# Performance work log

Measured on AMD Instinct MI355X. Metric: run time of the kernel, lower is better.

Reference implementation:

```python
import jax, jax.numpy as jnp
import numpy as np
import math

B, S, NV, D, VD = 2, 1024, 256, 4096, 768
H, KV, HD = 32, 4, 128
REP = H // KV
THETA, YSCALE, YALPHA, YBETA = 10000.0, 40.0, 1.0, 32.0
MAXSEQ = 2048
NEG = -1e30


def _yarn_cos_sin(n_pos):
    # YaRN-scaled RoPE tables, faithful to precompute_rope_yarn
    L_full = MAXSEQ * int(YSCALE)  # max_seq_len * yarn_scale as in __init__
    inv_freq = 1.0 / THETA ** (np.arange(0, HD, 2, dtype=np.float32) / HD)
    wavelengths = 2.0 * math.pi / inv_freq
    r = L_full / wavelengths
    gamma = np.clip((r - YALPHA) / (YBETA - YALPHA), 0.0, 1.0)
    inv_freq = inv_freq * ((1.0 - gamma) / YSCALE + gamma)
    freqs = np.outer(np.arange(n_pos, dtype=np.float32), inv_freq)
    emb = np.concatenate([freqs, freqs], axis=-1) / math.sqrt(0.1 * math.log(YSCALE) + 1.0)
    return jnp.asarray(np.cos(emb), jnp.float32), jnp.asarray(np.sin(emb), jnp.float32)


def setup_inputs() -> dict:
    key = jax.random.key(0)
    ks = jax.random.split(key, 7)
    x = jax.random.normal(ks[0], (B, S, D), jnp.float32)
    vision_features = jax.random.normal(ks[1], (B, NV, VD), jnp.float32)
    wq = jax.random.normal(ks[2], (H * HD, D), jnp.float32) * 0.02
    wk = jax.random.normal(ks[3], (KV * HD, D), jnp.float32) * 0.02
    wv = jax.random.normal(ks[4], (KV * HD, D), jnp.float32) * 0.02
    wo = jax.random.normal(ks[5], (D, H * HD), jnp.float32) * 0.02
    w_vision_kv = jax.random.normal(ks[6], (2 * KV * HD, VD), jnp.float32) * 0.02
    cos, sin = _yarn_cos_sin(S + NV)
    return {"x": x, "vision_features": vision_features, "wq": wq, "wk": wk,
            "wv": wv, "wo": wo, "w_vision_kv": w_vision_kv, "cos": cos, "sin": sin}


def _rotate_half(t):
    t1, t2 = t[..., : HD // 2], t[..., HD // 2 :]
    return jnp.concatenate([-t2, t1], axis=-1)


def reference(x, vision_features, wq, wk, wv, wo, w_vision_kv, cos, sin):
    b, s, _ = x.shape
    q = (x @ wq.T).reshape(b, s, H, HD)
    k = (x @ wk.T).reshape(b, s, KV, HD)
    v = (x @ wv.T).reshape(b, s, KV, HD)
    # vision KV prefix
    vkv = vision_features @ w_vision_kv.T  # [b, nv, 2*KV*HD]
    vk, vv = jnp.split(vkv, 2, axis=-1)
    nv = vision_features.shape[1]
    vk = vk.reshape(b, nv, KV, HD)
    vv = vv.reshape(b, nv, KV, HD)
    k = jnp.concatenate([vk, k], axis=1)  # [b, kvlen, KV, HD]
    v = jnp.concatenate([vv, v], axis=1)
    kvlen = k.shape[1]
    # RoPE (positions broadcast over heads)
    cq, sq = cos[None, :s, None, :], sin[None, :s, None, :]
    ck, sk = cos[None, :kvlen, None, :], sin[None, :kvlen, None, :]
    q = q * cq + _rotate_half(q) * sq
    k = k * ck + _rotate_half(k) * sk
    # GQA without materializing repeated K/V: group q heads by kv head
    qg = q.reshape(b, s, KV, REP, HD)
    scores = jnp.einsum("bsgrd,btgd->bgrst", qg, k) * (HD ** -0.5)
    # flash-style bottom-right causal: q pos i sees kv pos j <= i + (kvlen - s)
    i = jnp.arange(s)[:, None]
    j = jnp.arange(kvlen)[None, :]
    mask = j <= i + (kvlen - s)
    scores = jnp.where(mask, scores, NEG)
    probs = jax.nn.softmax(scores, axis=-1)
    out = jnp.einsum("bgrst,btgd->bsgrd", probs, v).reshape(b, s, H * HD)
    return out @ wo.T
```

## Files before the change

### kernel.cpp

```cpp
#include <hip/hip_runtime.h>
#include <hip/hip_bf16.h>
#include <cstdint>
#include <cstddef>

typedef short bf16x8 __attribute__((ext_vector_type(8)));
typedef float f32x4 __attribute__((ext_vector_type(4)));

__device__ __forceinline__ void gload_lds16(const void* g, void* l) {
  __builtin_amdgcn_global_load_lds((__attribute__((address_space(1))) const void*)g,
                                   (__attribute__((address_space(3))) void*)l, 16, 0, 0);
}

__device__ __forceinline__ unsigned short f2bf(float f) {
  unsigned u = __builtin_bit_cast(unsigned, f);
  u += 0x7fffu + ((u >> 16) & 1u);
  return (unsigned short)(u >> 16);
}
__device__ __forceinline__ float bf2f(unsigned short h) {
  unsigned u = ((unsigned)h) << 16;
  return __builtin_bit_cast(float, u);
}

struct CastPack {
  const float* s[7];
  unsigned short* d[7];
  int n4[7];
};
__global__ void k_cast_all(CastPack p) {
  const int tid0 = blockIdx.x * blockDim.x + threadIdx.x;
  const int stride = gridDim.x * blockDim.x;
#pragma unroll 1
  for (int seg = 0; seg < 7; ++seg) {
    const float4* __restrict__ src = reinterpret_cast<const float4*>(p.s[seg]);
    ushort4* __restrict__ dst = reinterpret_cast<ushort4*>(p.d[seg]);
    const int n4 = p.n4[seg];
    for (int i = tid0; i < n4; i += stride) {
      float4 v = src[i];
      ushort4 o;
      o.x = f2bf(v.x); o.y = f2bf(v.y); o.z = f2bf(v.z); o.w = f2bf(v.w);
      dst[i] = o;
    }
  }
}

__device__ __forceinline__ void storeC(float* C, size_t i, float v) { C[i] = v; }
__device__ __forceinline__ void storeC(unsigned short* C, size_t i, float v) { C[i] = f2bf(v); }

__global__ __launch_bounds__(256) void k_gemm_qv(
    const unsigned short* __restrict__ xb,
    const unsigned short* __restrict__ wqkvb,
    unsigned short* __restrict__ qkv,
    const unsigned short* __restrict__ visb,
    const unsigned short* __restrict__ wvkvb,
    unsigned short* __restrict__ vkvb) {
  __shared__ __align__(16) unsigned short lA[128 * 64];
  __shared__ __align__(16) unsigned short lB[128 * 64];
  const int tid = threadIdx.x;
  const int w = tid >> 6, l = tid & 63;
  const int orig = (int)blockIdx.x;
  const int tile = (orig & 7) * 84 + (orig >> 3);

  const unsigned short* A;
  const unsigned short* B;
  unsigned short* C;
  int K, N, m0, n0;
  if (tile < 640) {
    A = xb; B = wqkvb; C = qkv; K = 4096; N = 5120;
    m0 = (tile & 15) * 128;
    n0 = (tile >> 4) * 128;
  } else {
    int v = tile - 640;
    A = visb; B = wvkvb; C = vkvb; K = 768; N = 1024;
    m0 = (v & 3) * 128;
    n0 = (v >> 2) * 128;
  }
  const int wm = (w >> 1) * 64, wn = (w & 1) * 64;

  f32x4 acc[4][4];
#pragma unroll
  for (int i = 0; i < 4; ++i)
#pragma unroll
    for (int j = 0; j < 4; ++j) acc[i][j] = f32x4{0.f, 0.f, 0.f, 0.f};

  char* lAc = (char*)lA;
  char* lBc = (char*)lB;

  for (int k0 = 0; k0 < K; k0 += 64) {
#pragma unroll
    for (int p = 0; p < 4; ++p) {
      int r = (w * 4 + p) * 8 + (l >> 3);
      int c = (l & 7) ^ (r & 7);
      gload_lds16(A + (size_t)(m0 + r) * K + k0 + c * 8, lAc + (w * 4 + p) * 1024);
      gload_lds16(B + (size_t)(n0 + r) * K + k0 + c * 8, lBc + (w * 4 + p) * 1024);
    }
    __syncthreads();
#pragma unroll
    for (int kk = 0; kk < 2; ++kk) {
      bf16x8 af[4], bfr[4];
#pragma unroll
      for (int i = 0; i < 4; ++i) {
        int r = wm + i * 16 + (l & 15);
        int slot = (kk * 4 + (l >> 4)) ^ (r & 7);
        af[i] = *(const bf16x8*)(lAc + r * 128 + slot * 16);
      }
#pragma unroll
      for (int j = 0; j < 4; ++j) {
        int r = wn + j * 16 + (l & 15);
        int slot = (kk * 4 + (l >> 4)) ^ (r & 7);
        bfr[j] = *(const bf16x8*)(lBc + r * 128 + slot * 16);
      }
#pragma unroll
      for (int i = 0; i < 4; ++i)
#pragma unroll
        for (int j = 0; j < 4; ++j)
          acc[i][j] = __builtin_amdgcn_mfma_f32_16x16x32_bf16(af[i], bfr[j], acc[i][j], 0, 0, 0);
    }
    __syncthreads();
  }

#pragma unroll
  for (int i = 0; i < 4; ++i)
#pragma unroll
    for (int j = 0; j < 4; ++j) {
      int row = m0 + wm + i * 16 + (l >> 4) * 4;
      int col = n0 + wn + j * 16 + (l & 15);
#pragma unroll
      for (int r = 0; r < 4; ++r)
        storeC(C, (size_t)(row + r) * N + col, acc[i][j][r]);
    }
}

template <typename OutT>
__global__ __launch_bounds__(512) void k_gemm256x128(
    const unsigned short* __restrict__ A,
    const unsigned short* __restrict__ B,
    OutT* __restrict__ C,
    int M, int N, int K) {
  __shared__ __align__(16) unsigned short lA[2][2][256][32];
  __shared__ __align__(16) unsigned short lB[2][2][128][32];
  const int tid = threadIdx.x;
  const int w = tid >> 6, l = tid & 63;
  const int wr = w >> 2, wc = w & 3;
  const int lq = l & 15, g = l >> 4;
  const int fslot = (g ^ ((lq >> 1) & 3)) << 3;

  const int gm = M >> 8, gn = N >> 7;
  const int L = (int)blockIdx.x;
  const int xcd = L & 7, slot = L >> 3;
  const int m0 = (slot % gm) * 256;
  const int n0 = (xcd * (gn >> 3) + slot / gm) * 128;

  const unsigned short* Ap = A + (size_t)m0 * K;
  const unsigned short* Bp = B + (size_t)n0 * K;

  f32x4 acc[8][2];
#pragma unroll
  for (int i = 0; i < 8; ++i)
#pragma unroll
    for (int j = 0; j < 2; ++j) acc[i][j] = f32x4{0.f, 0.f, 0.f, 0.f};

  auto stageA = [&](unsigned short* lbase, int kcol) {
#pragma unroll
    for (int p = 0; p < 2; ++p) {
      int R = w * 32 + p * 16;
      int row = R + (l >> 2);
      int cc = ((l & 3) ^ ((l >> 3) & 3)) << 3;
      gload_lds16(Ap + (size_t)row * K + kcol + cc, lbase + R * 32);
    }
  };
  auto stageB = [&](unsigned short* lbase, int kcol) {
    int R = w * 16;
    int row = R + (l >> 2);
    int cc = ((l & 3) ^ ((l >> 3) & 3)) << 3;
    gload_lds16(Bp + (size_t)row * K + kcol + cc, lbase + R * 32);
  };

  const int nt = K >> 6;

  stageB(&lB[0][0][0][0], 0);
  stageA(&lA[0][0][0][0], 0);
  stageB(&lB[0][1][0][0], 32);
  stageA(&lA[0][1][0][0], 32);
  stageB(&lB[1][0][0][0], 64);
  stageA(&lA[1][0][0][0], 64);
  asm volatile("s_waitcnt vmcnt(3)" ::: "memory");
  __builtin_amdgcn_s_barrier();

  bf16x8 bfr[2], a[8];

  for (int T = 0; T < nt; ++T) {
    const int bf = T & 1, nb = bf ^ 1;

#pragma unroll
    for (int nf = 0; nf < 2; ++nf)
      bfr[nf] = *(const bf16x8*)&lB[bf][0][wc * 32 + nf * 16 + lq][fslot];
#pragma unroll
    for (int mf = 0; mf < 8; ++mf)
      a[mf] = *(const bf16x8*)&lA[bf][0][wr * 128 + mf * 16 + lq][fslot];
    if (T + 1 < nt) {
      stageA(&lA[nb][1][0][0], ((T + 1) << 6) + 32);
      stageB(&lB[nb][1][0][0], ((T + 1) << 6) + 32);
    }
    asm volatile("s_waitcnt lgkmcnt(0)" ::: "memory");
    __builtin_amdgcn_s_setprio(1);
#pragma unroll
    for (int mf = 0; mf < 8; ++mf)
#pragma unroll
      for (int nf = 0; nf < 2; ++nf)
        acc[mf][nf] = __builtin_amdgcn_mfma_f32_16x16x32_bf16(a[mf], bfr[nf], acc[mf][nf], 0, 0, 0);
    __builtin_amdgcn_s_setprio(0);
    __builtin_amdgcn_s_barrier();

#pragma unroll
    for (int nf = 0; nf < 2; ++nf)
      bfr[nf] = *(const bf16x8*)&lB[bf][1][wc * 32 + nf * 16 + lq][fslot];
#pragma unroll
    for (int mf = 0; mf < 8; ++mf)
      a[mf] = *(const bf16x8*)&lA[bf][1][wr * 128 + mf * 16 + lq][fslot];
    if (T + 2 < nt) {
      stageA(&lA[bf][0][0][0], (T + 2) << 6);
      stageB(&lB[bf][0][0][0], (T + 2) << 6);
    }
    asm volatile("s_waitcnt lgkmcnt(0)" ::: "memory");
    __builtin_amdgcn_s_setprio(1);
#pragma unroll
    for (int mf = 0; mf < 8; ++mf)
#pragma unroll
      for (int nf = 0; nf < 2; ++nf)
        acc[mf][nf] = __builtin_amdgcn_mfma_f32_16x16x32_bf16(a[mf], bfr[nf], acc[mf][nf], 0, 0, 0);
    __builtin_amdgcn_s_setprio(0);
    if (T < nt - 2)
      asm volatile("s_waitcnt vmcnt(3)" ::: "memory");
    else if (T == nt - 2)
      asm volatile("s_waitcnt vmcnt(0)" ::: "memory");
    __builtin_amdgcn_s_barrier();
  }

#pragma unroll
  for (int mf = 0; mf < 8; ++mf)
#pragma unroll
    for (int nf = 0; nf < 2; ++nf) {
      int row = m0 + wr * 128 + mf * 16 + g * 4;
      int col = n0 + wc * 32 + nf * 16 + lq;
#pragma unroll
      for (int r = 0; r < 4; ++r)
        storeC(C, (size_t)(row + r) * N + col, acc[mf][nf][r]);
    }
}

__global__ void k_post(const unsigned short* __restrict__ qkv,
                       const unsigned short* __restrict__ vkv,
                       const float* __restrict__ cosT, const float* __restrict__ sinT,
                       unsigned short* __restrict__ k_all,
                       unsigned short* __restrict__ v_t) {
  int idx = blockIdx.x * blockDim.x + threadIdx.x;
  if (idx < 655360) {
    int i = idx;
    int d0 = i & 63;
    int t = (i >> 6) % 1280;
    int bg = i / (64 * 1280);
    int b = bg >> 2, g = bg & 3;
    float a, bb;
    if (t < 256) {
      const unsigned short* src = vkv + (size_t)(b * 256 + t) * 1024 + g * 128;
      a = bf2f(src[d0]); bb = bf2f(src[d0 + 64]);
    } else {
      const unsigned short* src = qkv + (size_t)(b * 1024 + t - 256) * 5120 + 4096 + g * 128;
      a = bf2f(src[d0]); bb = bf2f(src[d0 + 64]);
    }
    float c0 = cosT[t * 128 + d0], s0 = sinT[t * 128 + d0];
    float c1 = cosT[t * 128 + d0 + 64], s1 = sinT[t * 128 + d0 + 64];
    unsigned short* dst = k_all + ((size_t)bg * 1280 + t) * 128;
    dst[d0] = f2bf(a * c0 - bb * s0);
    dst[d0 + 64] = f2bf(bb * c1 + a * s1);
  } else {
    int i = idx - 655360;
    int t = i % 1280;
    int d = (i / 1280) & 127;
    int bg = i / (1280 * 128);
    int b = bg >> 2, g = bg & 3;
    unsigned short v;
    if (t < 256) v = vkv[(size_t)(b * 256 + t) * 1024 + 512 + g * 128 + d];
    else         v = qkv[(size_t)(b * 1024 + t - 256) * 5120 + 4608 + g * 128 + d];
    v_t[(size_t)bg * 128 * 1280 + (size_t)d * 1280 + t] = v;
  }
}

__global__ __launch_bounds__(256) void k_attn(
    const unsigned short* __restrict__ qr,
    const unsigned short* __restrict__ k_all,
    const unsigned short* __restrict__ v_t,
    const float* __restrict__ cosT, const float* __restrict__ sinT,
    unsigned short* __restrict__ attn) {
  __shared__ __align__(16) unsigned short lK[2][64 * 128];
  __shared__ __align__(16) unsigned short lV[2][128 * 64];
  __shared__ __align__(16) unsigned short lPT[4][16][72];

  const int tid = threadIdx.x, w = tid >> 6, l = tid & 63;
  const int lq = l & 15, g = l >> 4;
  const int qpair = blockIdx.x;
  const int h = blockIdx.y, b = blockIdx.z;
  const int bg = b * 4 + (h >> 3);
  const unsigned short* kg = k_all + (size_t)bg * 1280 * 128;
  const unsigned short* vg = v_t + (size_t)bg * 128 * 1280;

  char* lKc = (char*)lK;
  char* lVc = (char*)lV;
  char* pbuf = (char*)&lPT[w][0][0];

  auto stage = [&](int t0, int bufsel) {
#pragma unroll
    for (int p = 0; p < 4; ++p) {
      int r = (w * 4 + p) * 4 + (l >> 4);
      int c = (l & 15) ^ (r & 7);
      gload_lds16(kg + (size_t)(t0 + r) * 128 + c * 8,
                  lKc + bufsel * 16384 + (w * 4 + p) * 1024);
    }
#pragma unroll
    for (int p = 0; p < 4; ++p) {
      int d = (w * 4 + p) * 8 + (l >> 3);
      int c = (l & 7) ^ (d & 7);
      gload_lds16(vg + (size_t)d * 1280 + t0 + c * 8,
                  lVc + bufsel * 16384 + (w * 4 + p) * 1024);
    }
  };

  int buf = 0;
#pragma unroll 1
  for (int half = 0; half < 2; ++half) {
    const int qb = (half ? (15 - qpair) : qpair) * 64;
    const int qrow_l = qb + w * 16 + lq;
    const int nIter = (qb + 320) >> 6;

    bf16x8 aq[4];
    {
      int row = qb + w * 16 + lq;
      const unsigned short* p = qr + (size_t)(b * 1024 + row) * 5120 + h * 128 + g * 8;
      bf16x8 r0 = *(const bf16x8*)(p);
      bf16x8 r1 = *(const bf16x8*)(p + 32);
      bf16x8 r2 = *(const bf16x8*)(p + 64);
      bf16x8 r3 = *(const bf16x8*)(p + 96);
      const float* cp = cosT + (size_t)row * 128;
      const float* sp = sinT + (size_t)row * 128;
      const float sc = 0.08838834764831845f;
#pragma unroll
      for (int j = 0; j < 8; ++j) {
        int d0 = g * 8 + j;
        float a0 = bf2f((unsigned short)r0[j]), b0 = bf2f((unsigned short)r2[j]);
        aq[0][j] = (short)f2bf((a0 * cp[d0] - b0 * sp[d0]) * sc);
        aq[2][j] = (short)f2bf((b0 * cp[d0 + 64] + a0 * sp[d0 + 64]) * sc);
        int d1 = 32 + g * 8 + j;
        float a1 = bf2f((unsigned short)r1[j]), b1 = bf2f((unsigned short)r3[j]);
        aq[1][j] = (short)f2bf((a1 * cp[d1] - b1 * sp[d1]) * sc);
        aq[3][j] = (short)f2bf((b1 * cp[d1 + 64] + a1 * sp[d1 + 64]) * sc);
      }
    }

    f32x4 o[8];
#pragma unroll
    for (int i = 0; i < 8; ++i) o[i] = f32x4{0.f, 0.f, 0.f, 0.f};
    float mr = -1e30f;
    float lrp = 0.f;

    stage(0, buf);
    __syncthreads();

    for (int it = 0; it < nIter; ++it) {
      const int t0 = it << 6;
      if (it + 1 < nIter) stage(t0 + 64, buf ^ 1);

      const char* kbase = lKc + buf * 16384;
      const char* vbase = lVc + buf * 16384;

      f32x4 sT[4];
#pragma unroll
      for (int sub = 0; sub < 4; ++sub) {
        f32x4 s4 = {0.f, 0.f, 0.f, 0.f};
        int krow = sub * 16 + lq;
        const char* kb = kbase + krow * 256;
#pragma unroll
        for (int kk = 0; kk < 4; ++kk) {
          int slot = (kk * 4 + g) ^ (krow & 7);
          bf16x8 kf = *(const bf16x8*)(kb + slot * 16);
          s4 = __builtin_amdgcn_mfma_f32_16x16x32_bf16(kf, aq[kk], s4, 0, 0, 0);
        }
        sT[sub] = s4;
      }

      if (t0 + 63 > qb + w * 16 + 256) {
#pragma unroll
        for (int sub = 0; sub < 4; ++sub)
#pragma unroll
          for (int r = 0; r < 4; ++r) {
            int t = t0 + sub * 16 + 4 * g + r;
            if (t > qrow_l + 256) sT[sub][r] = -1e30f;
          }
      }

      float pm = fmaxf(fmaxf(fmaxf(sT[0][0], sT[0][1]), fmaxf(sT[0][2], sT[0][3])),
                       fmaxf(fmaxf(sT[1][0], sT[1][1]), fmaxf(sT[1][2], sT[1][3])));
      pm = fmaxf(pm, fmaxf(fmaxf(fmaxf(sT[2][0], sT[2][1]), fmaxf(sT[2][2], sT[2][3])),
                           fmaxf(fmaxf(sT[3][0], sT[3][1]), fmaxf(sT[3][2], sT[3][3]))));
      pm = fmaxf(pm, __shfl_xor(pm, 16));
      pm = fmaxf(pm, __shfl_xor(pm, 32));

      if (!__all(pm <= mr + 8.0f)) {
        float mnew = fmaxf(mr, pm);
        float scl = __expf(mr - mnew);
        mr = mnew;
        lrp *= scl;
        float s0 = __shfl(scl, 4 * g + 0);
        float s1 = __shfl(scl, 4 * g + 1);
        float s2 = __shfl(scl, 4 * g + 2);
        float s3 = __shfl(scl, 4 * g + 3);
#pragma unroll
        for (int cs = 0; cs < 8; ++cs) {
          o[cs][0] *= s0; o[cs][1] *= s1; o[cs][2] *= s2; o[cs][3] *= s3;
        }
      }

#pragma unroll
      for (int sub = 0; sub < 4; ++sub) {
        float p0 = __expf(sT[sub][0] - mr);
        float p1 = __expf(sT[sub][1] - mr);
        float p2 = __expf(sT[sub][2] - mr);
        float p3 = __expf(sT[sub][3] - mr);
        lrp += (p0 + p1) + (p2 + p3);
        unsigned pk0, pk1;
        asm("v_cvt_pk_bf16_f32 %0, %1, %2" : "=v"(pk0) : "v"(p0), "v"(p1));
        asm("v_cvt_pk_bf16_f32 %0, %1, %2" : "=v"(pk1) : "v"(p2), "v"(p3));
        int c = (2 * sub + (g >> 1)) ^ (lq & 7);
        *(uint2*)(pbuf + lq * 144 + c * 16 + (g & 1) * 8) = make_uint2(pk0, pk1);
      }

      asm volatile("s_waitcnt lgkmcnt(0)" ::: "memory");

      bf16x8 pa0 = *(const bf16x8*)(pbuf + lq * 144 + ((g ^ (lq & 7)) * 16));
      bf16x8 pa1 = *(const bf16x8*)(pbuf + lq * 144 + (((4 + g) ^ (lq & 7)) * 16));

#pragma unroll
      for (int cs = 0; cs < 8; ++cs) {
        int drow = cs * 16 + lq;
        const char* vb = vbase + drow * 128;
        int s0i = g ^ (drow & 7);
        int s1i = (4 + g) ^ (drow & 7);
        bf16x8 v0 = *(const bf16x8*)(vb + s0i * 16);
        bf16x8 v1 = *(const bf16x8*)(vb + s1i * 16);
        o[cs] = __builtin_amdgcn_mfma_f32_16x16x32_bf16(pa0, v0, o[cs], 0, 0, 0);
        o[cs] = __builtin_amdgcn_mfma_f32_16x16x32_bf16(pa1, v1, o[cs], 0, 0, 0);
      }

      __syncthreads();
      buf ^= 1;
    }

    lrp += __shfl_xor(lrp, 16);
    lrp += __shfl_xor(lrp, 32);
    float inv = 1.0f / lrp;
    float invr[4];
    invr[0] = __shfl(inv, 4 * g + 0);
    invr[1] = __shfl(inv, 4 * g + 1);
    invr[2] = __shfl(inv, 4 * g + 2);
    invr[3] = __shfl(inv, 4 * g + 3);
#pragma unroll
    for (int cs = 0; cs < 8; ++cs)
#pragma unroll
      for (int r = 0; r < 4; ++r) {
        int row = qb + w * 16 + 4 * g + r;
        attn[(size_t)(b * 1024 + row) * 4096 + h * 128 + cs * 16 + lq] =
            f2bf(o[cs][r] * invr[r]);
      }
  }
}

extern "C" void kernel_launch(void* const* d_in, const int* in_sizes, int n_in,
                              void* d_out, int out_size, void* d_ws, size_t ws_size,
                              hipStream_t stream) {
  const float* x    = (const float*)d_in[0];
  const float* vis  = (const float*)d_in[1];
  const float* wq   = (const float*)d_in[2];
  const float* wk   = (const float*)d_in[3];
  const float* wv   = (const float*)d_in[4];
  const float* wo   = (const float*)d_in[5];
  const float* wvkv = (const float*)d_in[6];
  const float* cosT = (const float*)d_in[7];
  const float* sinT = (const float*)d_in[8];
  float* out = (float*)d_out;
  char* ws = (char*)d_ws;

  size_t off = 0;
  auto alloc = [&](size_t b) { size_t r = off; off += (b + 255) & ~(size_t)255; return r; };
  unsigned short* wqkvb = (unsigned short*)(ws + alloc((size_t)5120 * 4096 * 2));
  unsigned short* wob   = (unsigned short*)(ws + alloc((size_t)4096 * 4096 * 2));
  unsigned short* wvkvb = (unsigned short*)(ws + alloc((size_t)1024 * 768 * 2));
  unsigned short* visb  = (unsigned short*)(ws + alloc((size_t)512 * 768 * 2));
  unsigned short* xb    = (unsigned short*)(ws + alloc((size_t)2048 * 4096 * 2));
  unsigned short* qkv   = (unsigned short*)(ws + alloc((size_t)2048 * 5120 * 2));
  unsigned short* vkvb  = (unsigned short*)(ws + alloc((size_t)512 * 1024 * 2));
  unsigned short* kall  = (unsigned short*)(ws + alloc((size_t)8 * 1280 * 128 * 2));
  unsigned short* vt    = (unsigned short*)(ws + alloc((size_t)8 * 128 * 1280 * 2));
  unsigned short* attnb = xb;
  if (ws_size < off) return;

  CastPack cp;
  cp.s[0] = x;    cp.d[0] = xb;                           cp.n4[0] = 2048 * 4096 / 4;
  cp.s[1] = wq;   cp.d[1] = wqkvb;                        cp.n4[1] = 4096 * 4096 / 4;
  cp.s[2] = wk;   cp.d[2] = wqkvb + (size_t)4096 * 4096;  cp.n4[2] = 512 * 4096 / 4;
  cp.s[3] = wv;   cp.d[3] = wqkvb + (size_t)4608 * 4096;  cp.n4[3] = 512 * 4096 / 4;
  cp.s[4] = wo;   cp.d[4] = wob;                          cp.n4[4] = 4096 * 4096 / 4;
  cp.s[5] = wvkv; cp.d[5] = wvkvb;                        cp.n4[5] = 1024 * 768 / 4;
  cp.s[6] = vis;  cp.d[6] = visb;                         cp.n4[6] = 512 * 768 / 4;
  k_cast_all<<<dim3(2048), dim3(256), 0, stream>>>(cp);

  k_gemm_qv<<<dim3(672), dim3(256), 0, stream>>>(xb, wqkvb, qkv, visb, wvkvb, vkvb);

  k_post<<<dim3(7680), dim3(256), 0, stream>>>(qkv, vkvb, cosT, sinT, kall, vt);

  k_attn<<<dim3(8, 32, 2), dim3(256), 0, stream>>>(qkv, kall, vt, cosT, sinT, attnb);

  k_gemm256x128<float><<<dim3(256), dim3(512), 0, stream>>>(attnb, wob, out, 2048, 4096, 4096);
}
```

Baseline: 305.0 us.

## Share double-buffered 128x128 GEMM core across QKV and output projections

Adds a shared 128x128-tile GEMM routine with a split-K-half, double-buffered LDS pipeline built on async global-to-LDS loads, s_setprio and explicit vmcnt waits. The QKV/vision GEMM moves from its single-buffered loop with a full sync per k-step onto this routine. The output projection moves from 256x128 tiles with 512 threads to 128x128 tiles with 256 threads, giving 512 blocks for better occupancy and CU balance. Smaller tiles increase operand reloads from global memory for the output GEMM.

```diff
diff --git a/kernel.cpp b/kernel.cpp
--- a/kernel.cpp
+++ b/kernel.cpp
@@ -46,6 +46,107 @@
 __device__ __forceinline__ void storeC(float* C, size_t i, float v) { C[i] = v; }
 __device__ __forceinline__ void storeC(unsigned short* C, size_t i, float v) { C[i] = f2bf(v); }
 
+template <typename OutT>
+__device__ __forceinline__ void gemm128_run(
+    const unsigned short* __restrict__ Ap,
+    const unsigned short* __restrict__ Bp,
+    OutT* __restrict__ C, int K, int ldC, int m0, int n0,
+    unsigned short (&lA)[2][2][128][32], unsigned short (&lB)[2][2][128][32]) {
+  const int tid = threadIdx.x;
+  const int w = tid >> 6, l = tid & 63;
+  const int wr = w >> 1, wc = w & 1;
+  const int lq = l & 15, g = l >> 4;
+  const int fslot = (g ^ ((lq >> 1) & 3)) << 3;
+
+  f32x4 acc[4][4];
+#pragma unroll
+  for (int i = 0; i < 4; ++i)
+#pragma unroll
+    for (int j = 0; j < 4; ++j) acc[i][j] = f32x4{0.f, 0.f, 0.f, 0.f};
+
+  auto stageH = [&](const unsigned short* gbase, unsigned short* lbase, int kcol) {
+#pragma unroll
+    for (int p = 0; p < 2; ++p) {
+      int R = w * 32 + p * 16;
+      int row = R + (l >> 2);
+      int cc = ((l & 3) ^ ((l >> 3) & 3)) << 3;
+      gload_lds16(gbase + (size_t)row * K + kcol + cc, lbase + R * 32);
+    }
+  };
+
+  const int nt = K >> 6;
+
+  stageH(Bp, &lB[0][0][0][0], 0);
+  stageH(Ap, &lA[0][0][0][0], 0);
+  stageH(Bp, &lB[0][1][0][0], 32);
+  stageH(Ap, &lA[0][1][0][0], 32);
+  stageH(Bp, &lB[1][0][0][0], 64);
+  stageH(Ap, &lA[1][0][0][0], 64);
+  asm volatile("s_waitcnt vmcnt(4)" ::: "memory");
+  __builtin_amdgcn_s_barrier();
+
+  bf16x8 a[4], bq[4];
+
+  for (int T = 0; T < nt; ++T) {
+    const int bf = T & 1, nb = bf ^ 1;
+
+#pragma unroll
+    for (int i = 0; i < 4; ++i)
+      a[i] = *(const bf16x8*)&lA[bf][0][wr * 64 + i * 16 + lq][fslot];
+#pragma unroll
+    for (int j = 0; j < 4; ++j)
+      bq[j] = *(const bf16x8*)&lB[bf][0][wc * 64 + j * 16 + lq][fslot];
+    if (T + 1 < nt) {
+      stageH(Ap, &lA[nb][1][0][0], ((T + 1) << 6) + 32);
+      stageH(Bp, &lB[nb][1][0][0], ((T + 1) << 6) + 32);
+    }
+    asm volatile("s_waitcnt lgkmcnt(0)" ::: "memory");
+    __builtin_amdgcn_s_setprio(1);
+#pragma unroll
+    for (int i = 0; i < 4; ++i)
+#pragma unroll
+      for (int j = 0; j < 4; ++j)
+        acc[i][j] = __builtin_amdgcn_mfma_f32_16x16x32_bf16(a[i], bq[j], acc[i][j], 0, 0, 0);
+    __builtin_amdgcn_s_setprio(0);
+    __builtin_amdgcn_s_barrier();
+
+#pragma unroll
+    for (int i = 0; i < 4; ++i)
+      a[i] = *(const bf16x8*)&lA[bf][1][wr * 64 + i * 16 + lq][fslot];
+#pragma unroll
+    for (int j = 0; j < 4; ++j)
+      bq[j] = *(const bf16x8*)&lB[bf][1][wc * 64 + j * 16 + lq][fslot];
+    if (T + 2 < nt) {
+      stageH(Ap, &lA[bf][0][0][0], (T + 2) << 6);
+      stageH(Bp, &lB[bf][0][0][0], (T + 2) << 6);
+    }
+    asm volatile("s_waitcnt lgkmcnt(0)" ::: "memory");
+    __builtin_amdgcn_s_setprio(1);
+#pragma unroll
+    for (int i = 0; i < 4; ++i)
+#pragma unroll
+      for (int j = 0; j < 4; ++j)
+        acc[i][j] = __builtin_amdgcn_mfma_f32_16x16x32_bf16(a[i], bq[j], acc[i][j], 0, 0, 0);
+    __builtin_amdgcn_s_setprio(0);
+    if (T < nt - 2)
+      asm volatile("s_waitcnt vmcnt(4)" ::: "memory");
+    else if (T == nt - 2)
+      asm volatile("s_waitcnt vmcnt(0)" ::: "memory");
+    __builtin_amdgcn_s_barrier();
+  }
+
+#pragma unroll
+  for (int i = 0; i < 4; ++i)
+#pragma unroll
+    for (int j = 0; j < 4; ++j) {
+      int row = m0 + wr * 64 + i * 16 + g * 4;
+      int col = n0 + wc * 64 + j * 16 + lq;
+#pragma unroll
+      for (int r = 0; r < 4; ++r)
+        storeC(C, (size_t)(row + r) * ldC + col, acc[i][j][r]);
+    }
+}
+
 __global__ __launch_bounds__(256) void k_gemm_qv(
     const unsigned short* __restrict__ xb,
     const unsigned short* __restrict__ wqkvb,
@@ -53,199 +154,36 @@
     const unsigned short* __restrict__ visb,
     const unsigned short* __restrict__ wvkvb,
     unsigned short* __restrict__ vkvb) {
-  __shared__ __align__(16) unsigned short lA[128 * 64];
-  __shared__ __align__(16) unsigned short lB[128 * 64];
-  const int tid = threadIdx.x;
-  const int w = tid >> 6, l = tid & 63;
+  __shared__ __align__(16) unsigned short lA[2][2][128][32];
+  __shared__ __align__(16) unsigned short lB[2][2][128][32];
   const int orig = (int)blockIdx.x;
   const int tile = (orig & 7) * 84 + (orig >> 3);
-
-  const unsigned short* A;
-  const unsigned short* B;
-  unsigned short* C;
-  int K, N, m0, n0;
   if (tile < 640) {
-    A = xb; B = wqkvb; C = qkv; K = 4096; N = 5120;
-    m0 = (tile & 15) * 128;
-    n0 = (tile >> 4) * 128;
+    int m0 = (tile & 15) * 128;
+    int n0 = (tile >> 4) * 128;
+    gemm128_run<unsigned short>(xb + (size_t)m0 * 4096, wqkvb + (size_t)n0 * 4096,
+                                qkv, 4096, 5120, m0, n0, lA, lB);
   } else {
     int v = tile - 640;
-    A = visb; B = wvkvb; C = vkvb; K = 768; N = 1024;
-    m0 = (v & 3) * 128;
-    n0 = (v >> 2) * 128;
+    int m0 = (v & 3) * 128;
+    int n0 = (v >> 2) * 128;
+    gemm128_run<unsigned short>(visb + (size_t)m0 * 768, wvkvb + (size_t)n0 * 768,
+                                vkvb, 768, 1024, m0, n0, lA, lB);
   }
-  const int wm = (w >> 1) * 64, wn = (w & 1) * 64;
-
-  f32x4 acc[4][4];
-#pragma unroll
-  for (int i = 0; i < 4; ++i)
-#pragma unroll
-    for (int j = 0; j < 4; ++j) acc[i][j] = f32x4{0.f, 0.f, 0.f, 0.f};
-
-  char* lAc = (char*)lA;
-  char* lBc = (char*)lB;
-
-  for (int k0 = 0; k0 < K; k0 += 64) {
-#pragma unroll
-    for (int p = 0; p < 4; ++p) {
-      int r = (w * 4 + p) * 8 + (l >> 3);
-      int c = (l & 7) ^ (r & 7);
-      gload_lds16(A + (size_t)(m0 + r) * K + k0 + c * 8, lAc + (w * 4 + p) * 1024);
-      gload_lds16(B + (size_t)(n0 + r) * K + k0 + c * 8, lBc + (w * 4 + p) * 1024);
-    }
-    __syncthreads();
-#pragma unroll
-    for (int kk = 0; kk < 2; ++kk) {
-      bf16x8 af[4], bfr[4];
-#pragma unroll
-      for (int i = 0; i < 4; ++i) {
-        int r = wm + i * 16 + (l & 15);
-        int slot = (kk * 4 + (l >> 4)) ^ (r & 7);
-        af[i] = *(const bf16x8*)(lAc + r * 128 + slot * 16);
-      }
-#pragma unroll
-      for (int j = 0; j < 4; ++j) {
-        int r = wn + j * 16 + (l & 15);
-        int slot = (kk * 4 + (l >> 4)) ^ (r & 7);
-        bfr[j] = *(const bf16x8*)(lBc + r * 128 + slot * 16);
-      }
-#pragma unroll
-      for (int i = 0; i < 4; ++i)
-#pragma unroll
-        for (int j = 0; j < 4; ++j)
-          acc[i][j] = __builtin_amdgcn_mfma_f32_16x16x32_bf16(af[i], bfr[j], acc[i][j], 0, 0, 0);
-    }
-    __syncthreads();
-  }
-
-#pragma unroll
-  for (int i = 0; i < 4; ++i)
-#pragma unroll
-    for (int j = 0; j < 4; ++j) {
-      int row = m0 + wm + i * 16 + (l >> 4) * 4;
-      int col = n0 + wn + j * 16 + (l & 15);
-#pragma unroll
-      for (int r = 0; r < 4; ++r)
-        storeC(C, (size_t)(row + r) * N + col, acc[i][j][r]);
-    }
-}
-
-template <typename OutT>
-__global__ __launch_bounds__(512) void k_gemm256x128(
+}
+
+__global__ __launch_bounds__(256) void k_gemm_o(
     const unsigned short* __restrict__ A,
     const unsigned short* __restrict__ B,
-    OutT* __restrict__ C,
-    int M, int N, int K) {
-  __shared__ __align__(16) unsigned short lA[2][2][256][32];
+    float* __restrict__ C) {
+  __shared__ __align__(16) unsigned short lA[2][2][128][32];
   __shared__ __align__(16) unsigned short lB[2][2][128][32];
-  const int tid = threadIdx.x;
-  const int w = tid >> 6, l = tid & 63;
-  const int wr = w >> 2, wc = w & 3;
-  const int lq = l & 15, g = l >> 4;
-  const int fslot = (g ^ ((lq >> 1) & 3)) << 3;
-
-  const int gm = M >> 8, gn = N >> 7;
   const int L = (int)blockIdx.x;
   const int xcd = L & 7, slot = L >> 3;
-  const int m0 = (slot % gm) * 256;
-  const int n0 = (xcd * (gn >> 3) + slot / gm) * 128;
-
-  const unsigned short* Ap = A + (size_t)m0 * K;
-  const unsigned short* Bp = B + (size_t)n0 * K;
-
-  f32x4 acc[8][2];
-#pragma unroll
-  for (int i = 0; i < 8; ++i)
-#pragma unroll
-    for (int j = 0; j < 2; ++j) acc[i][j] = f32x4{0.f, 0.f, 0.f, 0.f};
-
-  auto stageA = [&](unsigned short* lbase, int kcol) {
-#pragma unroll
-    for (int p = 0; p < 2; ++p) {
-      int R = w * 32 + p * 16;
-      int row = R + (l >> 2);
-      int cc = ((l & 3) ^ ((l >> 3) & 3)) << 3;
-      gload_lds16(Ap + (size_t)row * K + kcol + cc, lbase + R * 32);
-    }
-  };
-  auto stageB = [&](unsigned short* lbase, int kcol) {
-    int R = w * 16;
-    int row = R + (l >> 2);
-    int cc = ((l & 3) ^ ((l >> 3) & 3)) << 3;
-    gload_lds16(Bp + (size_t)row * K + kcol + cc, lbase + R * 32);
-  };
-
-  const int nt = K >> 6;
-
-  stageB(&lB[0][0][0][0], 0);
-  stageA(&lA[0][0][0][0], 0);
-  stageB(&lB[0][1][0][0], 32);
-  stageA(&lA[0][1][0][0], 32);
-  stageB(&lB[1][0][0][0], 64);
-  stageA(&lA[1][0][0][0], 64);
-  asm volatile("s_waitcnt vmcnt(3)" ::: "memory");
-  __builtin_amdgcn_s_barrier();
-
-  bf16x8 bfr[2], a[8];
-
-  for (int T = 0; T < nt; ++T) {
-    const int bf = T & 1, nb = bf ^ 1;
-
-#pragma unroll
-    for (int nf = 0; nf < 2; ++nf)
-      bfr[nf] = *(const bf16x8*)&lB[bf][0][wc * 32 + nf * 16 + lq][fslot];
-#pragma unroll
-    for (int mf = 0; mf < 8; ++mf)
-      a[mf] = *(const bf16x8*)&lA[bf][0][wr * 128 + mf * 16 + lq][fslot];
-    if (T + 1 < nt) {
-      stageA(&lA[nb][1][0][0], ((T + 1) << 6) + 32);
-      stageB(&lB[nb][1][0][0], ((T + 1) << 6) + 32);
-    }
-    asm volatile("s_waitcnt lgkmcnt(0)" ::: "memory");
-    __builtin_amdgcn_s_setprio(1);
-#pragma unroll
-    for (int mf = 0; mf < 8; ++mf)
-#pragma unroll
-      for (int nf = 0; nf < 2; ++nf)
-        acc[mf][nf] = __builtin_amdgcn_mfma_f32_16x16x32_bf16(a[mf], bfr[nf], acc[mf][nf], 0, 0, 0);
-    __builtin_amdgcn_s_setprio(0);
-    __builtin_amdgcn_s_barrier();
-
-#pragma unroll
-    for (int nf = 0; nf < 2; ++nf)
-      bfr[nf] = *(const bf16x8*)&lB[bf][1][wc * 32 + nf * 16 + lq][fslot];
-#pragma unroll
-    for (int mf = 0; mf < 8; ++mf)
-      a[mf] = *(const bf16x8*)&lA[bf][1][wr * 128 + mf * 16 + lq][fslot];
-    if (T + 2 < nt) {
-      stageA(&lA[bf][0][0][0], (T + 2) << 6);
-      stageB(&lB[bf][0][0][0], (T + 2) << 6);
-    }
-    asm volatile("s_waitcnt lgkmcnt(0)" ::: "memory");
-    __builtin_amdgcn_s_setprio(1);
-#pragma unroll
-    for (int mf = 0; mf < 8; ++mf)
-#pragma unroll
-      for (int nf = 0; nf < 2; ++nf)
-        acc[mf][nf] = __builtin_amdgcn_mfma_f32_16x16x32_bf16(a[mf], bfr[nf], acc[mf][nf], 0, 0, 0);
-    __builtin_amdgcn_s_setprio(0);
-    if (T < nt - 2)
-      asm volatile("s_waitcnt vmcnt(3)" ::: "memory");
-    else if (T == nt - 2)
-      asm volatile("s_waitcnt vmcnt(0)" ::: "memory");
-    __builtin_amdgcn_s_barrier();
-  }
-
-#pragma unroll
-  for (int mf = 0; mf < 8; ++mf)
-#pragma unroll
-    for (int nf = 0; nf < 2; ++nf) {
-      int row = m0 + wr * 128 + mf * 16 + g * 4;
-      int col = n0 + wc * 32 + nf * 16 + lq;
-#pragma unroll
-      for (int r = 0; r < 4; ++r)
-        storeC(C, (size_t)(row + r) * N + col, acc[mf][nf][r]);
-    }
+  const int m0 = (slot & 15) * 128;
+  const int n0 = (xcd * 4 + (slot >> 4)) * 128;
+  gemm128_run<float>(A + (size_t)m0 * 4096, B + (size_t)n0 * 4096,
+                     C, 4096, 4096, m0, n0, lA, lB);
 }
 
 __global__ void k_post(const unsigned short* __restrict__ qkv,
@@ -518,5 +456,5 @@
 
   k_attn<<<dim3(8, 32, 2), dim3(256), 0, stream>>>(qkv, kall, vt, cosT, sinT, attnb);
 
-  k_gemm256x128<float><<<dim3(256), dim3(512), 0, stream>>>(attnb, wob, out, 2048, 4096, 4096);
-}
+  k_gemm_o<<<dim3(512), dim3(256), 0, stream>>>(attnb, wob, out);
+}
```

Result: slower. 328.7 us (+7.7%).
